# Kernel tuning notes

Measured on AMD Instinct MI355X. Metric: run time of the kernel, lower is better.

## Reference

```python
import jax, jax.numpy as jnp
import numpy as np

B, N, H, NB, NCT = 8, 4096, 1024, 128, 33
LN_EPS = 1e-5


def setup_inputs() -> dict:
    key = jax.random.key(0)
    ks = jax.random.split(key, 12)
    x = jax.random.normal(ks[0], (B, N, H), dtype=jnp.float32)
    cancer_type = jax.random.randint(ks[1], (B,), 0, NCT)
    block_ids = jax.random.randint(ks[2], (B, N), 0, NB)
    pad_mask = jnp.zeros((B, N), dtype=bool)
    s1 = 1.0 / np.sqrt(H)
    s2 = 1.0 / np.sqrt(H // 2)
    return {
        "x": x,
        "cancer_type": cancer_type,
        "block_ids": block_ids,
        "pad_mask": pad_mask,
        "W1": jax.random.normal(ks[3], (H, H // 2), jnp.float32) * s1,
        "b1": jnp.zeros((H // 2,), jnp.float32),
        "W2": jax.random.normal(ks[4], (H // 2, 1), jnp.float32) * s2,
        "b2": jnp.zeros((1,), jnp.float32),
        "ct_emb": jax.random.normal(ks[5], (NCT, NB), jnp.float32) * 0.1,
        "Wp": jax.random.normal(ks[6], (H, H), jnp.float32) * s1,
        "bp": jnp.zeros((H,), jnp.float32),
        "ln_g": jnp.ones((H,), jnp.float32),
        "ln_b": jnp.zeros((H,), jnp.float32),
    }


def reference(x, cancer_type, block_ids, pad_mask, W1, b1, W2, b2, ct_emb, Wp, bp, ln_g, ln_b):
    nb = ct_emb.shape[1]
    # gate MLP: (B,N)
    h = jnp.tanh(x @ W1 + b1)
    gate = (h @ W2 + b2)[..., 0]
    valid = ~pad_mask
    # block membership mask (B, NB, N)
    mask = (block_ids[:, None, :] == jnp.arange(nb)[None, :, None]) & valid[:, None, :]
    neg_inf = jnp.float32(-jnp.inf)
    scores = jnp.where(mask, gate[:, None, :], neg_inf)
    # stable masked softmax over N; empty blocks -> all-zero weights (nan_to_num(0))
    m = jnp.max(scores, axis=-1, keepdims=True)
    m = jnp.where(jnp.isfinite(m), m, 0.0)
    e = jnp.where(mask, jnp.exp(scores - m), 0.0)
    denom = jnp.sum(e, axis=-1, keepdims=True)
    w = jnp.where(denom > 0, e / jnp.maximum(denom, 1e-30), 0.0)
    # cancer-type modulation: weights * (1 + 0.1*ct_mod[:,bid])
    ct_mod = ct_emb[cancer_type]  # (B, NB)
    w = w * (1.0 + 0.1 * ct_mod)[:, :, None]
    # pooled per-block token (B, NB, H)
    pooled = jnp.einsum('bkn,bnh->bkh', w, x)
    # block_proj: Linear -> LayerNorm -> ELU (dropout = eval identity)
    y = pooled @ Wp + bp
    mu = jnp.mean(y, axis=-1, keepdims=True)
    var = jnp.mean((y - mu) ** 2, axis=-1, keepdims=True)
    y = (y - mu) * jax.lax.rsqrt(var + LN_EPS) * ln_g + ln_b
    y = jax.nn.elu(y)
    has_b = jnp.any(mask, axis=-1)              # (B, NB)
    present = jnp.any(has_b, axis=0)            # (NB,) torch loop skips blocks absent everywhere
    block_tokens = jnp.where(present[None, :, None], y, 0.0)
    return block_tokens, has_b
```

## Files before the change

kernel.cpp:

```cpp
#include <hip/hip_runtime.h>

#define NTOK 4096
#define HDIM 1024
#define HHALF 512
#define NBLK 128
#define CAP 256

typedef __attribute__((ext_vector_type(8))) short short8;
typedef __attribute__((ext_vector_type(4))) float f32x4;
typedef short bf16s;

__device__ __forceinline__ short f2bf(float f) {
    unsigned u = __builtin_bit_cast(unsigned, f);
    u = (u + 0x7fffu + ((u >> 16) & 1u)) >> 16;
    return (short)u;
}
__device__ __forceinline__ void gload_lds16(const void* g, void* l) {
    __builtin_amdgcn_global_load_lds(
        (const __attribute__((address_space(1))) unsigned int*)g,
        (__attribute__((address_space(3))) unsigned int*)l, 16, 0, 0);
}
__device__ __forceinline__ float fast_tanh(float v) {
    float e = __expf(2.0f * v);
    return 1.0f - 2.0f / (e + 1.0f);
}

__global__ void k_tcvt2(const float* __restrict__ W1, const float* __restrict__ Wp,
                        bf16s* __restrict__ w1t, bf16s* __restrict__ wpt) {
    __shared__ float tile[64][65];
    const int by = blockIdx.y;
    const float* in = (by < 8) ? W1 : Wp;
    bf16s* out = (by < 8) ? w1t : wpt;
    const int Nc = (by < 8) ? HHALF : HDIM;
    const int n0 = ((by < 8) ? by : (by - 8)) * 64;
    const int k0 = blockIdx.x * 64;
    const int tx = threadIdx.x & 63, ty = threadIdx.x >> 6;
    #pragma unroll
    for (int i = 0; i < 16; ++i) {
        int r = ty + i * 4;
        tile[r][tx] = in[(size_t)(k0 + r) * Nc + n0 + tx];
    }
    __syncthreads();
    #pragma unroll
    for (int i = 0; i < 16; ++i) {
        int r = ty + i * 4;
        out[(size_t)(n0 + r) * 1024 + k0 + tx] = f2bf(tile[tx][r]);
    }
}

__global__ __launch_bounds__(256, 3) void k_gemm_h(
    const float* __restrict__ x, const bf16s* __restrict__ w1t,
    const float* __restrict__ b1, const float* __restrict__ w2,
    float* __restrict__ partial)
{
    __shared__ alignas(16) bf16s As[128 * 36];
    __shared__ alignas(16) bf16s Bs[128 * 32];
    __shared__ float gp[2][128];

    const int tid = threadIdx.x;
    const int lane = tid & 63;
    const int wv = tid >> 6;
    const int wr = wv >> 1, wc = wv & 1;
    const int phys = blockIdx.x;
    const int logical = (phys & 7) * 128 + (phys >> 3);
    const int row0 = (logical >> 2) * 128;
    const int col0 = (logical & 3) * 128;
    const int c0 = lane & 15, khalf = lane >> 4;

    const int ar = tid >> 1, ah = tid & 1;
    const float* xsrc = &x[(size_t)(row0 + ar) * HDIM + ah * 16];

    const int brow = wv * 32 + (lane >> 2);
    const int bj = lane & 3;

    f32x4 acc[4][4] = {};
    float4 pa0 = *reinterpret_cast<const float4*>(xsrc);
    float4 pa1 = *reinterpret_cast<const float4*>(xsrc + 4);
    float4 pa2 = *reinterpret_cast<const float4*>(xsrc + 8);
    float4 pa3 = *reinterpret_cast<const float4*>(xsrc + 12);

    for (int t = 0; t < 32; ++t) {
        const int kt = t * 32;
        __syncthreads();
        {
            short h[16] = {f2bf(pa0.x), f2bf(pa0.y), f2bf(pa0.z), f2bf(pa0.w),
                           f2bf(pa1.x), f2bf(pa1.y), f2bf(pa1.z), f2bf(pa1.w),
                           f2bf(pa2.x), f2bf(pa2.y), f2bf(pa2.z), f2bf(pa2.w),
                           f2bf(pa3.x), f2bf(pa3.y), f2bf(pa3.z), f2bf(pa3.w)};
            *reinterpret_cast<int4*>(&As[ar * 36 + ah * 16]) =
                *reinterpret_cast<const int4*>(&h[0]);
            *reinterpret_cast<int4*>(&As[ar * 36 + ah * 16 + 8]) =
                *reinterpret_cast<const int4*>(&h[8]);
        }
        #pragma unroll
        for (int q = 0; q < 2; ++q) {
            int r = brow + q * 16;
            int j = bj ^ ((r >> 1) & 3);
            gload_lds16(&w1t[(size_t)(col0 + r) * HDIM + kt + j * 8],
                        &Bs[(wv * 32 + q * 16) * 32 + lane * 8]);
        }
        __syncthreads();
        if (t < 31) {
            pa0 = *reinterpret_cast<const float4*>(xsrc + kt + 32);
            pa1 = *reinterpret_cast<const float4*>(xsrc + kt + 36);
            pa2 = *reinterpret_cast<const float4*>(xsrc + kt + 40);
            pa3 = *reinterpret_cast<const float4*>(xsrc + kt + 44);
        }
        const int kk = khalf * 8;
        short8 av[4];
        #pragma unroll
        for (int mf = 0; mf < 4; ++mf)
            av[mf] = *reinterpret_cast<const short8*>(
                &As[(wr * 64 + mf * 16 + c0) * 36 + kk]);
        #pragma unroll
        for (int nf = 0; nf < 4; ++nf) {
            int rb = wc * 64 + nf * 16 + c0;
            short8 bv = *reinterpret_cast<const short8*>(
                &Bs[rb * 32 + ((khalf ^ ((rb >> 1) & 3)) * 8)]);
            #pragma unroll
            for (int mf = 0; mf < 4; ++mf)
                acc[mf][nf] = __builtin_amdgcn_mfma_f32_16x16x32_bf16(av[mf], bv, acc[mf][nf], 0, 0, 0);
        }
    }

    float b1v[4], w2v[4];
    #pragma unroll
    for (int nf = 0; nf < 4; ++nf) {
        int gc = col0 + wc * 64 + nf * 16 + c0;
        b1v[nf] = b1[gc];
        w2v[nf] = w2[gc];
    }
    #pragma unroll
    for (int mf = 0; mf < 4; ++mf) {
        #pragma unroll
        for (int reg = 0; reg < 4; ++reg) {
            float s = 0.f;
            #pragma unroll
            for (int nf = 0; nf < 4; ++nf)
                s += fast_tanh(acc[mf][nf][reg] + b1v[nf]) * w2v[nf];
            s += __shfl_xor(s, 1); s += __shfl_xor(s, 2);
            s += __shfl_xor(s, 4); s += __shfl_xor(s, 8);
            if (c0 == 0) gp[wc][wr * 64 + mf * 16 + khalf * 4 + reg] = s;
        }
    }
    __syncthreads();
    if (tid < 128)
        partial[(size_t)(logical & 3) * 32768 + row0 + tid] = gp[0][tid] + gp[1][tid];
}

__global__ void k_gate_sum(const float* __restrict__ partial, const float* __restrict__ b2,
                           float* __restrict__ gate) {
    int i = (blockIdx.x * 256 + threadIdx.x) * 4;
    float4 p0 = *reinterpret_cast<const float4*>(&partial[i]);
    float4 p1 = *reinterpret_cast<const float4*>(&partial[32768 + i]);
    float4 p2 = *reinterpret_cast<const float4*>(&partial[65536 + i]);
    float4 p3 = *reinterpret_cast<const float4*>(&partial[98304 + i]);
    float bb = b2[0];
    float4 o = {p0.x + p1.x + p2.x + p3.x + bb, p0.y + p1.y + p2.y + p3.y + bb,
                p0.z + p1.z + p2.z + p3.z + bb, p0.w + p1.w + p2.w + p3.w + bb};
    *reinterpret_cast<float4*>(&gate[i]) = o;
}

__global__ void k_blocks(const int* __restrict__ block_ids, const unsigned char* __restrict__ pad,
                         const float* __restrict__ gate, const int* __restrict__ ct,
                         const float* __restrict__ ct_emb,
                         int* __restrict__ counts, float* __restrict__ mblk,
                         float* __restrict__ wscale, int* __restrict__ lists,
                         float* __restrict__ out_hasb)
{
    const int blk = blockIdx.x;
    const int b = blk >> 7, k = blk & 127;
    const int lane = threadIdx.x;
    const int base = b * NTOK;
    const int lbase = blk * CAP;
    const unsigned long long ltmask = (1ull << lane) - 1ull;

    float m = -__builtin_inff();
    float s = 0.f;
    int pos = 0;
    for (int t0 = 0; t0 < NTOK; t0 += 64) {
        int t = t0 + lane;
        bool mt = (block_ids[base + t] == k) && (pad[base + t] == 0);
        float g = gate[base + t];
        unsigned long long mask = __ballot(mt);
        if (mt) {
            int my = pos + __popcll(mask & ltmask);
            if (my < CAP) lists[lbase + my] = t;
            float mn = fmaxf(m, g);
            s = s * __expf(m - mn) + __expf(g - mn);
            m = mn;
        }
        pos += __popcll(mask);
    }
    #pragma unroll
    for (int off = 1; off < 64; off <<= 1) {
        float om = __shfl_xor(m, off);
        float os = __shfl_xor(s, off);
        float mn = fmaxf(m, om);
        float sa = (m == -__builtin_inff()) ? 0.f : s * __expf(m - mn);
        float sb = (om == -__builtin_inff()) ? 0.f : os * __expf(om - mn);
        s = sa + sb;
        m = mn;
    }
    if (lane == 0) {
        counts[blk] = pos;
        mblk[blk] = (pos > 0) ? m : 0.f;
        float mod = 1.0f + 0.1f * ct_emb[ct[b] * NBLK + k];
        wscale[blk] = (pos > 0 && s > 0.f) ? (mod / fmaxf(s, 1e-30f)) : 0.f;
        out_hasb[blk] = (pos > 0) ? 1.f : 0.f;
    }
}

__global__ void k_pool(const float* __restrict__ x, const float* __restrict__ gate,
                       const int* __restrict__ lists, const int* __restrict__ counts,
                       const float* __restrict__ mblk, const float* __restrict__ wscale,
                       bf16s* __restrict__ pooled)
{
    const int blk = blockIdx.x;
    const int b = blk >> 7;
    const int tid = threadIdx.x;
    const int base = b * NTOK;
    const int cnt = min(counts[blk], CAP);
    const int lbase = blk * CAP;
    const float m = mblk[blk], ws = wscale[blk];

    float4 acc = {0.f, 0.f, 0.f, 0.f};
    for (int i = 0; i < cnt; ++i) {
        int n = lists[lbase + i];
        float w = __expf(gate[base + n] - m);
        float4 xv = *reinterpret_cast<const float4*>(&x[(size_t)(base + n) * HDIM + tid * 4]);
        acc.x += w * xv.x; acc.y += w * xv.y; acc.z += w * xv.z; acc.w += w * xv.w;
    }
    short o[4] = {f2bf(acc.x * ws), f2bf(acc.y * ws), f2bf(acc.z * ws), f2bf(acc.w * ws)};
    *reinterpret_cast<int2*>(&pooled[(size_t)blk * HDIM + tid * 4]) =
        *reinterpret_cast<const int2*>(o);
}

__global__ __launch_bounds__(256) void k_gemm2(
    const bf16s* __restrict__ pooled, const bf16s* __restrict__ wpt,
    const float* __restrict__ bp, float* __restrict__ y)
{
    __shared__ alignas(16) bf16s As[2][64 * 32];
    __shared__ alignas(16) bf16s Bs[2][64 * 32];
    const int tid = threadIdx.x;
    const int lane = tid & 63;
    const int wv = tid >> 6;
    const int wr = wv >> 1, wc = wv & 1;
    const int row0 = (blockIdx.x >> 4) * 64, col0 = (blockIdx.x & 15) * 64;
    const int c0 = lane & 15, khalf = lane >> 4;

    const int sr = wv * 16 + (lane >> 2);
    const int sj = (lane & 3) ^ ((sr >> 1) & 3);
    const int sdst = (wv * 16) * 32 + lane * 8;
    const bf16s* srcA = &pooled[(size_t)(row0 + sr) * 1024 + sj * 8];
    const bf16s* srcB = &wpt[(size_t)(col0 + sr) * 1024 + sj * 8];

    f32x4 acc[2][2] = {};

    gload_lds16(srcA, &As[0][sdst]);
    gload_lds16(srcB, &Bs[0][sdst]);
    __syncthreads();

    for (int t = 0; t < 32; ++t) {
        const int cur = t & 1;
        if (t < 31) {
            gload_lds16(srcA + (t + 1) * 32, &As[cur ^ 1][sdst]);
            gload_lds16(srcB + (t + 1) * 32, &Bs[cur ^ 1][sdst]);
        }
        #pragma unroll
        for (int mf = 0; mf < 2; ++mf) {
            int ra = wr * 32 + mf * 16 + c0;
            short8 av = *reinterpret_cast<const short8*>(
                &As[cur][ra * 32 + ((khalf ^ ((ra >> 1) & 3)) * 8)]);
            #pragma unroll
            for (int nf = 0; nf < 2; ++nf) {
                int rb = wc * 32 + nf * 16 + c0;
                short8 bv = *reinterpret_cast<const short8*>(
                    &Bs[cur][rb * 32 + ((khalf ^ ((rb >> 1) & 3)) * 8)]);
                acc[mf][nf] = __builtin_amdgcn_mfma_f32_16x16x32_bf16(av, bv, acc[mf][nf], 0, 0, 0);
            }
        }
        __syncthreads();
    }
    #pragma unroll
    for (int mf = 0; mf < 2; ++mf)
        #pragma unroll
        for (int nf = 0; nf < 2; ++nf)
            #pragma unroll
            for (int reg = 0; reg < 4; ++reg) {
                int grow = row0 + wr * 32 + mf * 16 + khalf * 4 + reg;
                int gcol = col0 + wc * 32 + nf * 16 + c0;
                y[(size_t)grow * 1024 + gcol] = acc[mf][nf][reg] + bp[gcol];
            }
}

__global__ void k_lnelu(const float* __restrict__ y, const float* __restrict__ ln_g,
                        const float* __restrict__ ln_b, const int* __restrict__ counts,
                        float* __restrict__ outp)
{
    const int row = blockIdx.x;
    const int k = row & 127;
    const int tid = threadIdx.x;

    float4 v = *reinterpret_cast<const float4*>(&y[(size_t)row * 1024 + tid * 4]);
    float s = v.x + v.y + v.z + v.w;
    float ss = v.x * v.x + v.y * v.y + v.z * v.z + v.w * v.w;
    #pragma unroll
    for (int off = 32; off; off >>= 1) { s += __shfl_xor(s, off); ss += __shfl_xor(ss, off); }

    __shared__ float sbuf[4], ssbuf[4];
    int wv = tid >> 6;
    if ((tid & 63) == 0) { sbuf[wv] = s; ssbuf[wv] = ss; }
    __syncthreads();
    s = sbuf[0] + sbuf[1] + sbuf[2] + sbuf[3];
    ss = ssbuf[0] + ssbuf[1] + ssbuf[2] + ssbuf[3];

    float mu = s * (1.f / 1024.f);
    float var = ss * (1.f / 1024.f) - mu * mu;
    float rstd = rsqrtf(var + 1e-5f);

    bool pres = false;
    #pragma unroll
    for (int bb = 0; bb < 8; ++bb) pres = pres || (counts[bb * NBLK + k] > 0);

    float4 g4 = *reinterpret_cast<const float4*>(&ln_g[tid * 4]);
    float4 b4 = *reinterpret_cast<const float4*>(&ln_b[tid * 4]);
    float vals[4] = {v.x, v.y, v.z, v.w};
    float gs[4] = {g4.x, g4.y, g4.z, g4.w};
    float bs[4] = {b4.x, b4.y, b4.z, b4.w};
    float4 o;
    float* op = &o.x;
    #pragma unroll
    for (int j = 0; j < 4; ++j) {
        float t = (vals[j] - mu) * rstd * gs[j] + bs[j];
        t = (t > 0.f) ? t : expm1f(t);
        op[j] = pres ? t : 0.f;
    }
    *reinterpret_cast<float4*>(&outp[(size_t)row * 1024 + tid * 4]) = o;
}

extern "C" void kernel_launch(void* const* d_in, const int* in_sizes, int n_in,
                              void* d_out, int out_size, void* d_ws, size_t ws_size,
                              hipStream_t stream)
{
    const float* x      = (const float*)d_in[0];
    const int*   ct     = (const int*)d_in[1];
    const int*   bids   = (const int*)d_in[2];
    const unsigned char* pad = (const unsigned char*)d_in[3];
    const float* W1     = (const float*)d_in[4];
    const float* b1     = (const float*)d_in[5];
    const float* W2     = (const float*)d_in[6];
    const float* b2     = (const float*)d_in[7];
    const float* ct_emb = (const float*)d_in[8];
    const float* Wp     = (const float*)d_in[9];
    const float* bp     = (const float*)d_in[10];
    const float* ln_g   = (const float*)d_in[11];
    const float* ln_b   = (const float*)d_in[12];
    float* outF = (float*)d_out;

    char* ws = (char*)d_ws;
    bf16s* w1t    = (bf16s*)(ws + 0);
    bf16s* wpt    = (bf16s*)(ws + 1048576);
    float* gate   = (float*)(ws + 3145728);
    float* part   = (float*)(ws + 3276800);
    float* mblk   = (float*)(ws + 3801088);
    float* wscal  = (float*)(ws + 3805184);
    int*   counts = (int*)  (ws + 3809280);
    int*   lists  = (int*)  (ws + 3813376);
    bf16s* pooled = (bf16s*)(ws + 4861952);
    float* ybuf   = (float*)(ws + 6959104);

    k_tcvt2<<<dim3(16, 24), 256, 0, stream>>>(W1, Wp, w1t, wpt);
    k_gemm_h<<<1024, 256, 0, stream>>>(x, w1t, b1, W2, part);
    k_gate_sum<<<32, 256, 0, stream>>>(part, b2, gate);
    k_blocks<<<1024, 64, 0, stream>>>(bids, pad, gate, ct, ct_emb, counts, mblk, wscal,
                                      lists, outF + (size_t)8 * NBLK * HDIM);
    k_pool<<<1024, 256, 0, stream>>>(x, gate, lists, counts, mblk, wscal, pooled);
    k_gemm2<<<256, 256, 0, stream>>>(pooled, wpt, bp, ybuf);
    k_lnelu<<<1024, 256, 0, stream>>>(ybuf, ln_g, ln_b, counts, outF);
}
```

Before: 142.8 us.

## Pre-convert x to bf16 and use direct-to-LDS loads in gate GEMM

Adds a pass that converts x to a bf16 copy in workspace. The gate GEMM then streams A tiles with global_load_lds and a swizzled layout instead of converting fp32 in registers, and the pooling kernel reads the bf16 copy. The extra pass costs a full fp32 read plus a bf16 write of x before the GEMM. In return it removes per-tile conversion work and halves the bytes read by later consumers. The new path runs only when the workspace is large enough, otherwise it falls back to the old kernel.

```diff
diff --git a/kernel.cpp b/kernel.cpp
--- a/kernel.cpp
+++ b/kernel.cpp
@@ -5,6 +5,7 @@
 #define HHALF 512
 #define NBLK 128
 #define CAP 256
+#define XELEMS 33554432ull
 
 typedef __attribute__((ext_vector_type(8))) short short8;
 typedef __attribute__((ext_vector_type(4))) float f32x4;
@@ -23,6 +24,17 @@
 __device__ __forceinline__ float fast_tanh(float v) {
     float e = __expf(2.0f * v);
     return 1.0f - 2.0f / (e + 1.0f);
+}
+
+__global__ void k_xcvt(const float* __restrict__ in, bf16s* __restrict__ out) {
+    for (size_t i = ((size_t)blockIdx.x * 256 + threadIdx.x) * 8; i < XELEMS;
+         i += (size_t)gridDim.x * 256 * 8) {
+        float4 a = *reinterpret_cast<const float4*>(&in[i]);
+        float4 b = *reinterpret_cast<const float4*>(&in[i + 4]);
+        short h[8] = {f2bf(a.x), f2bf(a.y), f2bf(a.z), f2bf(a.w),
+                      f2bf(b.x), f2bf(b.y), f2bf(b.z), f2bf(b.w)};
+        *reinterpret_cast<int4*>(&out[i]) = *reinterpret_cast<const int4*>(h);
+    }
 }
 
 __global__ void k_tcvt2(const float* __restrict__ W1, const float* __restrict__ Wp,
@@ -48,12 +60,12 @@
     }
 }
 
-__global__ __launch_bounds__(256, 3) void k_gemm_h(
-    const float* __restrict__ x, const bf16s* __restrict__ w1t,
+__global__ __launch_bounds__(256, 4) void k_gemm_g(
+    const bf16s* __restrict__ xb, const bf16s* __restrict__ w1t,
     const float* __restrict__ b1, const float* __restrict__ w2,
     float* __restrict__ partial)
 {
-    __shared__ alignas(16) bf16s As[128 * 36];
+    __shared__ alignas(16) bf16s As[128 * 32];
     __shared__ alignas(16) bf16s Bs[128 * 32];
     __shared__ float gp[2][128];
 
@@ -67,9 +79,89 @@
     const int col0 = (logical & 3) * 128;
     const int c0 = lane & 15, khalf = lane >> 4;
 
+    const int srow = wv * 32 + (lane >> 2);
+    const int sj = lane & 3;
+
+    f32x4 acc[4][4] = {};
+
+    for (int t = 0; t < 32; ++t) {
+        const int kt = t * 32;
+        __syncthreads();
+        #pragma unroll
+        for (int q = 0; q < 2; ++q) {
+            int r = srow + q * 16;
+            int j = sj ^ ((r >> 1) & 3);
+            gload_lds16(&xb[(size_t)(row0 + r) * HDIM + kt + j * 8],
+                        &As[(wv * 32 + q * 16) * 32 + lane * 8]);
+            gload_lds16(&w1t[(size_t)(col0 + r) * HDIM + kt + j * 8],
+                        &Bs[(wv * 32 + q * 16) * 32 + lane * 8]);
+        }
+        __syncthreads();
+        const int kk = khalf;
+        short8 av[4];
+        #pragma unroll
+        for (int mf = 0; mf < 4; ++mf) {
+            int ra = wr * 64 + mf * 16 + c0;
+            av[mf] = *reinterpret_cast<const short8*>(
+                &As[ra * 32 + ((kk ^ ((ra >> 1) & 3)) * 8)]);
+        }
+        #pragma unroll
+        for (int nf = 0; nf < 4; ++nf) {
+            int rb = wc * 64 + nf * 16 + c0;
+            short8 bv = *reinterpret_cast<const short8*>(
+                &Bs[rb * 32 + ((kk ^ ((rb >> 1) & 3)) * 8)]);
+            #pragma unroll
+            for (int mf = 0; mf < 4; ++mf)
+                acc[mf][nf] = __builtin_amdgcn_mfma_f32_16x16x32_bf16(av[mf], bv, acc[mf][nf], 0, 0, 0);
+        }
+    }
+
+    float b1v[4], w2v[4];
+    #pragma unroll
+    for (int nf = 0; nf < 4; ++nf) {
+        int gc = col0 + wc * 64 + nf * 16 + c0;
+        b1v[nf] = b1[gc];
+        w2v[nf] = w2[gc];
+    }
+    #pragma unroll
+    for (int mf = 0; mf < 4; ++mf) {
+        #pragma unroll
+        for (int reg = 0; reg < 4; ++reg) {
+            float s = 0.f;
+            #pragma unroll
+            for (int nf = 0; nf < 4; ++nf)
+                s += fast_tanh(acc[mf][nf][reg] + b1v[nf]) * w2v[nf];
+            s += __shfl_xor(s, 1); s += __shfl_xor(s, 2);
+            s += __shfl_xor(s, 4); s += __shfl_xor(s, 8);
+            if (c0 == 0) gp[wc][wr * 64 + mf * 16 + khalf * 4 + reg] = s;
+        }
+    }
+    __syncthreads();
+    if (tid < 128)
+        partial[(size_t)(logical & 3) * 32768 + row0 + tid] = gp[0][tid] + gp[1][tid];
+}
+
+__global__ __launch_bounds__(256, 3) void k_gemm_h(
+    const float* __restrict__ x, const bf16s* __restrict__ w1t,
+    const float* __restrict__ b1, const float* __restrict__ w2,
+    float* __restrict__ partial)
+{
+    __shared__ alignas(16) bf16s As[128 * 36];
+    __shared__ alignas(16) bf16s Bs[128 * 32];
+    __shared__ float gp[2][128];
+
+    const int tid = threadIdx.x;
+    const int lane = tid & 63;
+    const int wv = tid >> 6;
+    const int wr = wv >> 1, wc = wv & 1;
+    const int phys = blockIdx.x;
+    const int logical = (phys & 7) * 128 + (phys >> 3);
+    const int row0 = (logical >> 2) * 128;
+    const int col0 = (logical & 3) * 128;
+    const int c0 = lane & 15, khalf = lane >> 4;
+
     const int ar = tid >> 1, ah = tid & 1;
     const float* xsrc = &x[(size_t)(row0 + ar) * HDIM + ah * 16];
-
     const int brow = wv * 32 + (lane >> 2);
     const int bj = lane & 3;
 
@@ -122,7 +214,6 @@
                 acc[mf][nf] = __builtin_amdgcn_mfma_f32_16x16x32_bf16(av[mf], bv, acc[mf][nf], 0, 0, 0);
         }
     }
-
     float b1v[4], w2v[4];
     #pragma unroll
     for (int nf = 0; nf < 4; ++nf) {
@@ -211,7 +302,8 @@
     }
 }
 
-__global__ void k_pool(const float* __restrict__ x, const float* __restrict__ gate,
+__global__ void k_pool(const float* __restrict__ x, const bf16s* __restrict__ xb, int use_bf,
+                       const float* __restrict__ gate,
                        const int* __restrict__ lists, const int* __restrict__ counts,
                        const float* __restrict__ mblk, const float* __restrict__ wscale,
                        bf16s* __restrict__ pooled)
@@ -228,7 +320,20 @@
     for (int i = 0; i < cnt; ++i) {
         int n = lists[lbase + i];
         float w = __expf(gate[base + n] - m);
-        float4 xv = *reinterpret_cast<const float4*>(&x[(size_t)(base + n) * HDIM + tid * 4]);
+        float4 xv;
+        if (use_bf) {
+            int2 rv = *reinterpret_cast<const int2*>(&xb[(size_t)(base + n) * HDIM + tid * 4]);
+            short s4[4];
+            *reinterpret_cast<int2*>(s4) = rv;
+            unsigned u0 = ((unsigned)(unsigned short)s4[0]) << 16;
+            unsigned u1 = ((unsigned)(unsigned short)s4[1]) << 16;
+            unsigned u2 = ((unsigned)(unsigned short)s4[2]) << 16;
+            unsigned u3 = ((unsigned)(unsigned short)s4[3]) << 16;
+            xv.x = __builtin_bit_cast(float, u0); xv.y = __builtin_bit_cast(float, u1);
+            xv.z = __builtin_bit_cast(float, u2); xv.w = __builtin_bit_cast(float, u3);
+        } else {
+            xv = *reinterpret_cast<const float4*>(&x[(size_t)(base + n) * HDIM + tid * 4]);
+        }
         acc.x += w * xv.x; acc.y += w * xv.y; acc.z += w * xv.z; acc.w += w * xv.w;
     }
     short o[4] = {f2bf(acc.x * ws), f2bf(acc.y * ws), f2bf(acc.z * ws), f2bf(acc.w * ws)};
@@ -369,13 +474,20 @@
     int*   lists  = (int*)  (ws + 3813376);
     bf16s* pooled = (bf16s*)(ws + 4861952);
     float* ybuf   = (float*)(ws + 6959104);
+    bf16s* xb     = (bf16s*)(ws + 11153408);
+    const int use_xb = (ws_size >= 78262272ull) ? 1 : 0;
 
     k_tcvt2<<<dim3(16, 24), 256, 0, stream>>>(W1, Wp, w1t, wpt);
-    k_gemm_h<<<1024, 256, 0, stream>>>(x, w1t, b1, W2, part);
+    if (use_xb) {
+        k_xcvt<<<2048, 256, 0, stream>>>(x, xb);
+        k_gemm_g<<<1024, 256, 0, stream>>>(xb, w1t, b1, W2, part);
+    } else {
+        k_gemm_h<<<1024, 256, 0, stream>>>(x, w1t, b1, W2, part);
+    }
     k_gate_sum<<<32, 256, 0, stream>>>(part, b2, gate);
     k_blocks<<<1024, 64, 0, stream>>>(bids, pad, gate, ct, ct_emb, counts, mblk, wscal,
                                       lists, outF + (size_t)8 * NBLK * HDIM);
-    k_pool<<<1024, 256, 0, stream>>>(x, gate, lists, counts, mblk, wscal, pooled);
+    k_pool<<<1024, 256, 0, stream>>>(x, xb, use_xb, gate, lists, counts, mblk, wscal, pooled);
     k_gemm2<<<256, 256, 0, stream>>>(pooled, wpt, bp, ybuf);
     k_lnelu<<<1024, 256, 0, stream>>>(ybuf, ln_g, ln_b, counts, outF);
 }
```

Result: slower. 159.7 us (+11.8%).

## Double-buffer gate GEMM with async fp32 LDS loads and fold gate sum into block pass

Applied to the files above, without the earlier changes.

The gate GEMM now streams fp32 x tiles straight into double-buffered LDS with global_load_lds and converts them to bf16 at fragment-read time. Explicit vmcnt waits and raw barriers overlap the next tile's loads with the current MFMAs, and the MFMA section runs at raised priority. The separate gate-sum kernel is removed: k_blocks adds the four partials plus bias for its member tokens and writes gate itself, saving a launch and one pass over the partials. k_gemm2 gets the same waitcnt/barrier pipelining. In exchange LDS use grows (the fp32 A tile doubles its footprint) and each A element is converted to bf16 more than once.

```diff
diff --git a/kernel.cpp b/kernel.cpp
--- a/kernel.cpp
+++ b/kernel.cpp
@@ -48,13 +48,13 @@
     }
 }
 
-__global__ __launch_bounds__(256, 3) void k_gemm_h(
+__global__ __launch_bounds__(256, 3) void k_gemm_gf(
     const float* __restrict__ x, const bf16s* __restrict__ w1t,
     const float* __restrict__ b1, const float* __restrict__ w2,
     float* __restrict__ partial)
 {
-    __shared__ alignas(16) bf16s As[128 * 36];
-    __shared__ alignas(16) bf16s Bs[128 * 32];
+    __shared__ alignas(16) float As[2][128 * 32];
+    __shared__ alignas(16) bf16s Bs[2][128 * 32];
     __shared__ float gp[2][128];
 
     const int tid = threadIdx.x;
@@ -67,60 +67,72 @@
     const int col0 = (logical & 3) * 128;
     const int c0 = lane & 15, khalf = lane >> 4;
 
-    const int ar = tid >> 1, ah = tid & 1;
-    const float* xsrc = &x[(size_t)(row0 + ar) * HDIM + ah * 16];
-
-    const int brow = wv * 32 + (lane >> 2);
-    const int bj = lane & 3;
+    const int aRow = wv * 32 + (lane >> 3);
+    const int aj = (lane & 7) ^ ((lane >> 3) & 7);
+    const float* aSrc = &x[(size_t)(row0 + aRow) * HDIM + aj * 4];
+    const int adst = wv * 1024 + lane * 4;
+
+    const int bRow = wv * 32 + (lane >> 2);
+    const int bj = (lane & 3) ^ ((lane >> 3) & 3);
+    const bf16s* bSrc = &w1t[(size_t)(col0 + bRow) * HDIM + bj * 8];
+    const int bdst = wv * 1024 + lane * 8;
 
     f32x4 acc[4][4] = {};
-    float4 pa0 = *reinterpret_cast<const float4*>(xsrc);
-    float4 pa1 = *reinterpret_cast<const float4*>(xsrc + 4);
-    float4 pa2 = *reinterpret_cast<const float4*>(xsrc + 8);
-    float4 pa3 = *reinterpret_cast<const float4*>(xsrc + 12);
+
+    #pragma unroll
+    for (int q = 0; q < 4; ++q)
+        gload_lds16(aSrc + q * 8 * HDIM, &As[0][adst + q * 256]);
+    #pragma unroll
+    for (int q = 0; q < 2; ++q)
+        gload_lds16(bSrc + q * 16 * HDIM, &Bs[0][bdst + q * 512]);
 
     for (int t = 0; t < 32; ++t) {
-        const int kt = t * 32;
-        __syncthreads();
-        {
-            short h[16] = {f2bf(pa0.x), f2bf(pa0.y), f2bf(pa0.z), f2bf(pa0.w),
-                           f2bf(pa1.x), f2bf(pa1.y), f2bf(pa1.z), f2bf(pa1.w),
-                           f2bf(pa2.x), f2bf(pa2.y), f2bf(pa2.z), f2bf(pa2.w),
-                           f2bf(pa3.x), f2bf(pa3.y), f2bf(pa3.z), f2bf(pa3.w)};
-            *reinterpret_cast<int4*>(&As[ar * 36 + ah * 16]) =
-                *reinterpret_cast<const int4*>(&h[0]);
-            *reinterpret_cast<int4*>(&As[ar * 36 + ah * 16 + 8]) =
-                *reinterpret_cast<const int4*>(&h[8]);
-        }
-        #pragma unroll
-        for (int q = 0; q < 2; ++q) {
-            int r = brow + q * 16;
-            int j = bj ^ ((r >> 1) & 3);
-            gload_lds16(&w1t[(size_t)(col0 + r) * HDIM + kt + j * 8],
-                        &Bs[(wv * 32 + q * 16) * 32 + lane * 8]);
-        }
-        __syncthreads();
+        const int cur = t & 1;
         if (t < 31) {
-            pa0 = *reinterpret_cast<const float4*>(xsrc + kt + 32);
-            pa1 = *reinterpret_cast<const float4*>(xsrc + kt + 36);
-            pa2 = *reinterpret_cast<const float4*>(xsrc + kt + 40);
-            pa3 = *reinterpret_cast<const float4*>(xsrc + kt + 44);
-        }
-        const int kk = khalf * 8;
-        short8 av[4];
-        #pragma unroll
-        for (int mf = 0; mf < 4; ++mf)
-            av[mf] = *reinterpret_cast<const short8*>(
-                &As[(wr * 64 + mf * 16 + c0) * 36 + kk]);
+            const int ko = (t + 1) * 32;
+            #pragma unroll
+            for (int q = 0; q < 4; ++q)
+                gload_lds16(aSrc + q * 8 * HDIM + ko, &As[cur ^ 1][adst + q * 256]);
+            #pragma unroll
+            for (int q = 0; q < 2; ++q)
+                gload_lds16(bSrc + q * 16 * HDIM + ko, &Bs[cur ^ 1][bdst + q * 512]);
+            asm volatile("s_waitcnt vmcnt(6)" ::: "memory");
+        } else {
+            asm volatile("s_waitcnt vmcnt(0)" ::: "memory");
+        }
+        __builtin_amdgcn_s_barrier();
+        __builtin_amdgcn_sched_barrier(0);
+
+        short8 av[4], bv[4];
+        #pragma unroll
+        for (int mf = 0; mf < 4; ++mf) {
+            int ra = wr * 64 + mf * 16 + c0;
+            f32x4 lo = *reinterpret_cast<const f32x4*>(
+                &As[cur][ra * 32 + (((2 * khalf) ^ (ra & 7)) * 4)]);
+            f32x4 hi = *reinterpret_cast<const f32x4*>(
+                &As[cur][ra * 32 + (((2 * khalf + 1) ^ (ra & 7)) * 4)]);
+            short h[8] = {f2bf(lo[0]), f2bf(lo[1]), f2bf(lo[2]), f2bf(lo[3]),
+                          f2bf(hi[0]), f2bf(hi[1]), f2bf(hi[2]), f2bf(hi[3])};
+            av[mf] = *reinterpret_cast<const short8*>(h);
+        }
         #pragma unroll
         for (int nf = 0; nf < 4; ++nf) {
             int rb = wc * 64 + nf * 16 + c0;
-            short8 bv = *reinterpret_cast<const short8*>(
-                &Bs[rb * 32 + ((khalf ^ ((rb >> 1) & 3)) * 8)]);
+            bv[nf] = *reinterpret_cast<const short8*>(
+                &Bs[cur][rb * 32 + ((khalf ^ ((rb >> 1) & 3)) * 8)]);
+        }
+
+        __builtin_amdgcn_s_setprio(1);
+        #pragma unroll
+        for (int nf = 0; nf < 4; ++nf)
             #pragma unroll
             for (int mf = 0; mf < 4; ++mf)
-                acc[mf][nf] = __builtin_amdgcn_mfma_f32_16x16x32_bf16(av[mf], bv, acc[mf][nf], 0, 0, 0);
-        }
+                acc[mf][nf] = __builtin_amdgcn_mfma_f32_16x16x32_bf16(av[mf], bv[nf], acc[mf][nf], 0, 0, 0);
+        __builtin_amdgcn_s_setprio(0);
+
+        asm volatile("s_waitcnt lgkmcnt(0)" ::: "memory");
+        __builtin_amdgcn_sched_barrier(0);
+        __builtin_amdgcn_s_barrier();
     }
 
     float b1v[4], w2v[4];
@@ -148,21 +160,9 @@
         partial[(size_t)(logical & 3) * 32768 + row0 + tid] = gp[0][tid] + gp[1][tid];
 }
 
-__global__ void k_gate_sum(const float* __restrict__ partial, const float* __restrict__ b2,
-                           float* __restrict__ gate) {
-    int i = (blockIdx.x * 256 + threadIdx.x) * 4;
-    float4 p0 = *reinterpret_cast<const float4*>(&partial[i]);
-    float4 p1 = *reinterpret_cast<const float4*>(&partial[32768 + i]);
-    float4 p2 = *reinterpret_cast<const float4*>(&partial[65536 + i]);
-    float4 p3 = *reinterpret_cast<const float4*>(&partial[98304 + i]);
-    float bb = b2[0];
-    float4 o = {p0.x + p1.x + p2.x + p3.x + bb, p0.y + p1.y + p2.y + p3.y + bb,
-                p0.z + p1.z + p2.z + p3.z + bb, p0.w + p1.w + p2.w + p3.w + bb};
-    *reinterpret_cast<float4*>(&gate[i]) = o;
-}
-
 __global__ void k_blocks(const int* __restrict__ block_ids, const unsigned char* __restrict__ pad,
-                         const float* __restrict__ gate, const int* __restrict__ ct,
+                         const float* __restrict__ part, const float* __restrict__ b2,
+                         float* __restrict__ gate, const int* __restrict__ ct,
                          const float* __restrict__ ct_emb,
                          int* __restrict__ counts, float* __restrict__ mblk,
                          float* __restrict__ wscale, int* __restrict__ lists,
@@ -174,6 +174,7 @@
     const int base = b * NTOK;
     const int lbase = blk * CAP;
     const unsigned long long ltmask = (1ull << lane) - 1ull;
+    const float b2v = b2[0];
 
     float m = -__builtin_inff();
     float s = 0.f;
@@ -181,9 +182,11 @@
     for (int t0 = 0; t0 < NTOK; t0 += 64) {
         int t = t0 + lane;
         bool mt = (block_ids[base + t] == k) && (pad[base + t] == 0);
-        float g = gate[base + t];
         unsigned long long mask = __ballot(mt);
         if (mt) {
+            int r = base + t;
+            float g = part[r] + part[32768 + r] + part[65536 + r] + part[98304 + r] + b2v;
+            gate[r] = g;
             int my = pos + __popcll(mask & ltmask);
             if (my < CAP) lists[lbase + my] = t;
             float mn = fmaxf(m, g);
@@ -259,14 +262,18 @@
 
     gload_lds16(srcA, &As[0][sdst]);
     gload_lds16(srcB, &Bs[0][sdst]);
-    __syncthreads();
 
     for (int t = 0; t < 32; ++t) {
         const int cur = t & 1;
         if (t < 31) {
             gload_lds16(srcA + (t + 1) * 32, &As[cur ^ 1][sdst]);
             gload_lds16(srcB + (t + 1) * 32, &Bs[cur ^ 1][sdst]);
-        }
+            asm volatile("s_waitcnt vmcnt(2)" ::: "memory");
+        } else {
+            asm volatile("s_waitcnt vmcnt(0)" ::: "memory");
+        }
+        __builtin_amdgcn_s_barrier();
+        __builtin_amdgcn_sched_barrier(0);
         #pragma unroll
         for (int mf = 0; mf < 2; ++mf) {
             int ra = wr * 32 + mf * 16 + c0;
@@ -280,7 +287,9 @@
                 acc[mf][nf] = __builtin_amdgcn_mfma_f32_16x16x32_bf16(av, bv, acc[mf][nf], 0, 0, 0);
             }
         }
-        __syncthreads();
+        asm volatile("s_waitcnt lgkmcnt(0)" ::: "memory");
+        __builtin_amdgcn_sched_barrier(0);
+        __builtin_amdgcn_s_barrier();
     }
     #pragma unroll
     for (int mf = 0; mf < 2; ++mf)
@@ -371,10 +380,10 @@
     float* ybuf   = (float*)(ws + 6959104);
 
     k_tcvt2<<<dim3(16, 24), 256, 0, stream>>>(W1, Wp, w1t, wpt);
-    k_gemm_h<<<1024, 256, 0, stream>>>(x, w1t, b1, W2, part);
-    k_gate_sum<<<32, 256, 0, stream>>>(part, b2, gate);
-    k_blocks<<<1024, 64, 0, stream>>>(bids, pad, gate, ct, ct_emb, counts, mblk, wscal,
-                                      lists, outF + (size_t)8 * NBLK * HDIM);
+    k_gemm_gf<<<1024, 256, 0, stream>>>(x, w1t, b1, W2, part);
+    k_blocks<<<1024, 64, 0, stream>>>(bids, pad, part, b2, gate, ct, ct_emb,
+                                      counts, mblk, wscal, lists,
+                                      outF + (size_t)8 * NBLK * HDIM);
     k_pool<<<1024, 256, 0, stream>>>(x, gate, lists, counts, mblk, wscal, pooled);
     k_gemm2<<<256, 256, 0, stream>>>(pooled, wpt, bp, ybuf);
     k_lnelu<<<1024, 256, 0, stream>>>(ybuf, ln_g, ln_b, counts, outF);
```

Result: slower. 151.8 us (+6.3%).
